# Kernel tuning notes

Measured on AMD Instinct MI355X. Metric: run time of the kernel, lower is better.

The kernel has to match this reference:

```python
import jax, jax.numpy as jnp
import numpy as np

B, F, D = 1024, 160000, 16


def setup_inputs() -> dict:
    key = jax.random.key(0)
    k1, k2, k3 = jax.random.split(key, 3)
    x = jax.random.randint(k1, (B, F), 0, 2, dtype=jnp.int32)  # multi-hot transaction
    emb_w = jax.random.normal(k2, (F, D), dtype=jnp.float32) * 0.05  # FM factor table
    bias_w = jax.random.normal(k3, (F, 1), dtype=jnp.float32) * 0.05  # per-field linear bias
    g_bias = jnp.zeros((), dtype=jnp.float32)  # global bias
    return {"x": x, "emb_w": emb_w, "bias_w": bias_w, "g_bias": g_bias}


def reference(x, emb_w, bias_w, g_bias):
    # mask[b,f] = 1 where field f is active (row > 0 in original tf code)
    mask = (x > 0).astype(emb_w.dtype)  # [B, F]
    # sum of active embeddings per row: equals gather+sum in the original
    ev = mask @ emb_w  # [B, D]
    # sum of squared norms of active embeddings per row
    rowsq = jnp.sum(emb_w * emb_w, axis=1)  # [F]
    sum_sq = mask @ rowsq  # [B]
    # 0.5 * (sum_{i,j} e_i . e_j - sum_i ||e_i||^2) == FM pairwise interaction
    second = 0.5 * (jnp.sum(ev * ev, axis=-1) - sum_sq)  # [B]
    # linear term: global bias + sum of active field biases
    linear = g_bias + mask @ bias_w  # [B, 1]
    return linear + second[:, None]  # [B, 1]
```

## Files before the change

### kernel.cpp

```cpp
#include <hip/hip_runtime.h>
#include <hip/hip_bf16.h>

#define B_ROWS 1024
#define F_FLD  160000
#define D_DIM  16
#define NKB    (F_FLD / 32)
#define NSTAT  (D_DIM + 1)
#define ACC_N  (B_ROWS * NSTAT)
#define CCOLS  6400
#define NGRP   (CCOLS / 256)
#define KBC    (CCOLS / 32)
#define NCHUNK (F_FLD / CCOLS)
#define ROWS_B 16
#define WAVES  8

typedef __attribute__((ext_vector_type(8))) short bf16x8;
typedef __attribute__((ext_vector_type(4))) float f32x4;

static __device__ inline unsigned short f2bf(float x) {
    __hip_bfloat16 h = __float2bfloat16(x);
    union { __hip_bfloat16 h; unsigned short s; } u; u.h = h; return u.s;
}

static __device__ inline bf16x8 expand8(unsigned b) {
    union { unsigned u[4]; bf16x8 v; } r;
    r.u[0] = ((b        & 1u) * 0x3F80u) | (((b >> 1) & 1u) * 0x3F800000u);
    r.u[1] = (((b >> 2) & 1u) * 0x3F80u) | (((b >> 3) & 1u) * 0x3F800000u);
    r.u[2] = (((b >> 4) & 1u) * 0x3F80u) | (((b >> 5) & 1u) * 0x3F800000u);
    r.u[3] = (((b >> 6) & 1u) * 0x3F80u) | (((b >> 7) & 1u) * 0x3F800000u);
    return r.v;
}

__global__ __launch_bounds__(256) void fm_pack(const float* __restrict__ emb,
                                               const float* __restrict__ bias,
                                               unsigned short* __restrict__ embB,
                                               unsigned short* __restrict__ cB2c,
                                               float* __restrict__ acc) {
    const int tid = threadIdx.x;
    const int kb = blockIdx.x * 4 + (tid >> 6);
    const int l = tid & 63, q = l >> 4, n = l & 15;

    float e[8];
    union { unsigned short s[8]; uint4 u; } v;
#pragma unroll
    for (int j = 0; j < 8; ++j) {
        int f = kb * 32 + 4 * j + q;
        e[j] = emb[(size_t)f * D_DIM + n];
        v.s[j] = f2bf(e[j]);
    }
    *(uint4*)(embB + ((size_t)kb * 64 + l) * 8) = v.u;

    union { unsigned short s[8]; uint4 u; } w;
#pragma unroll
    for (int j = 0; j < 8; ++j) {
        float s = e[j] * e[j];
        s += __shfl_xor(s, 1);
        s += __shfl_xor(s, 2);
        s += __shfl_xor(s, 4);
        s += __shfl_xor(s, 8);
        int f = kb * 32 + 4 * j + q;
        w.s[j] = f2bf((n == 0 ? bias[f] : 0.0f) - 0.5f * s);
    }
    if (n == 0) *(uint4*)(cB2c + ((size_t)kb * 4 + q) * 8) = w.u;

    int gid = blockIdx.x * 256 + tid;
    if (gid < ACC_N) acc[gid] = 0.0f;
}

__global__ __launch_bounds__(512, 6) void fm_main(const int* __restrict__ x,
                                                  const unsigned short* __restrict__ embB,
                                                  const unsigned short* __restrict__ cB2c,
                                                  float* __restrict__ acc) {
    __shared__ unsigned long long msk[NGRP][ROWS_B][4];
    __shared__ float red[WAVES][ROWS_B][NSTAT];

    const int tid = threadIdx.x;
    const int w = tid >> 6, l = tid & 63;
    const int q = l >> 4, n = l & 15;
    const int rowbase = blockIdx.y * ROWS_B;
    const int c0 = blockIdx.x * CCOLS;

#pragma unroll
    for (int rr = 0; rr < 2; ++rr) {
        const int rloc = 2 * w + rr;
        const int4* xp = (const int4*)(x + (size_t)(rowbase + rloc) * F_FLD + c0) + l;
        for (int g0 = 0; g0 < NGRP; g0 += 5) {
            int4 v[5];
#pragma unroll
            for (int k = 0; k < 5; ++k) v[k] = xp[(size_t)(g0 + k) * 64];
#pragma unroll
            for (int k = 0; k < 5; ++k) {
                unsigned long long m0 = __ballot(v[k].x > 0);
                unsigned long long m1 = __ballot(v[k].y > 0);
                unsigned long long m2 = __ballot(v[k].z > 0);
                unsigned long long m3 = __ballot(v[k].w > 0);
                if (l == 0) {
                    msk[g0 + k][rloc][0] = m0; msk[g0 + k][rloc][1] = m1;
                    msk[g0 + k][rloc][2] = m2; msk[g0 + k][rloc][3] = m3;
                }
            }
        }
    }
    __syncthreads();

    f32x4 aev = {0.f, 0.f, 0.f, 0.f}, ac = {0.f, 0.f, 0.f, 0.f};
    const uint4* eB = (const uint4*)embB;
    const uint4* cB = (const uint4*)cB2c;
    const int kbg0 = blockIdx.x * KBC;

#pragma unroll 2
    for (int t = 0; t < KBC / WAVES; ++t) {
        const int kb = w * (KBC / WAVES) + t;
        const int g = kb >> 3, byt = kb & 7;
        unsigned long long mv = msk[g][n][q];
        unsigned b = (unsigned)(mv >> (8 * byt)) & 0xFFu;
        bf16x8 A = expand8(b);
        union { uint4 u; bf16x8 v; } Bf, Cf;
        Bf.u = eB[(size_t)(kbg0 + kb) * 64 + l];
        Cf.u = cB[(size_t)(kbg0 + kb) * 4 + q];
        aev = __builtin_amdgcn_mfma_f32_16x16x32_bf16(A, Bf.v, aev, 0, 0, 0);
        ac  = __builtin_amdgcn_mfma_f32_16x16x32_bf16(A, Cf.v, ac,  0, 0, 0);
    }

#pragma unroll
    for (int r = 0; r < 4; ++r) {
        red[w][q * 4 + r][n] = aev[r];
        if (n == 0) red[w][q * 4 + r][16] = ac[r];
    }
    __syncthreads();

    if (tid < ROWS_B * NSTAT) {
        int row = tid / NSTAT, col = tid % NSTAT;
        float s = 0.0f;
#pragma unroll
        for (int ww = 0; ww < WAVES; ++ww) s += red[ww][row][col];
        atomicAdd(acc + (size_t)(rowbase + row) * NSTAT + col, s);
    }
}

__global__ __launch_bounds__(256) void fm_final(const float* __restrict__ acc,
                                                const float* __restrict__ g_bias,
                                                float* __restrict__ out) {
    int row = blockIdx.x * 256 + threadIdx.x;
    if (row >= B_ROWS) return;
    const float* a = acc + (size_t)row * NSTAT;
    float s = 0.0f;
#pragma unroll
    for (int d = 0; d < D_DIM; ++d) s += a[d] * a[d];
    out[row] = g_bias[0] + a[16] + 0.5f * s;
}

extern "C" void kernel_launch(void* const* d_in, const int* in_sizes, int n_in,
                              void* d_out, int out_size, void* d_ws, size_t ws_size,
                              hipStream_t stream) {
    const int*   x      = (const int*)d_in[0];
    const float* emb_w  = (const float*)d_in[1];
    const float* bias_w = (const float*)d_in[2];
    const float* g_bias = (const float*)d_in[3];
    float*       out    = (float*)d_out;

    unsigned short* embB = (unsigned short*)d_ws;
    unsigned short* cB2c = (unsigned short*)((char*)d_ws + (size_t)NKB * 64 * 8 * 2);
    float*          acc  = (float*)((char*)d_ws + (size_t)NKB * 64 * 8 * 2
                                                + (size_t)NKB * 4 * 8 * 2);

    fm_pack<<<dim3(NKB / 4), dim3(256), 0, stream>>>(emb_w, bias_w, embB, cB2c, acc);
    fm_main<<<dim3(NCHUNK, B_ROWS / ROWS_B), dim3(512), 0, stream>>>(x, embB, cB2c, acc);
    fm_final<<<dim3((B_ROWS + 255) / 256), dim3(256), 0, stream>>>(acc, g_bias, out);
}
```

Before: 849.5 us.

## Split mask packing into its own kernel and tile GEMM over 64 rows

The fused kernel is split into two. One kernel reads x with software-prefetched loads and writes packed bitmasks to global memory. A separate GEMM kernel processes 64 rows per block, so each embedding tile is reused across four times as many rows. The atomic accumulation is replaced by per-chunk partial sums that the final kernel reduces, which removes the accumulator zeroing and the atomics. The cost is an extra launch plus a round trip of the mask and partials through global memory.

```diff
diff --git a/kernel.cpp b/kernel.cpp
--- a/kernel.cpp
+++ b/kernel.cpp
@@ -6,13 +6,11 @@
 #define D_DIM  16
 #define NKB    (F_FLD / 32)
 #define NSTAT  (D_DIM + 1)
-#define ACC_N  (B_ROWS * NSTAT)
 #define CCOLS  6400
 #define NGRP   (CCOLS / 256)
 #define KBC    (CCOLS / 32)
 #define NCHUNK (F_FLD / CCOLS)
-#define ROWS_B 16
-#define WAVES  8
+#define MSTRIDE 101
 
 typedef __attribute__((ext_vector_type(8))) short bf16x8;
 typedef __attribute__((ext_vector_type(4))) float f32x4;
@@ -34,8 +32,7 @@
 __global__ __launch_bounds__(256) void fm_pack(const float* __restrict__ emb,
                                                const float* __restrict__ bias,
                                                unsigned short* __restrict__ embB,
-                                               unsigned short* __restrict__ cB2c,
-                                               float* __restrict__ acc) {
+                                               unsigned short* __restrict__ cB2c) {
     const int tid = threadIdx.x;
     const int kb = blockIdx.x * 4 + (tid >> 6);
     const int l = tid & 63, q = l >> 4, n = l & 15;
@@ -62,43 +59,64 @@
         w.s[j] = f2bf((n == 0 ? bias[f] : 0.0f) - 0.5f * s);
     }
     if (n == 0) *(uint4*)(cB2c + ((size_t)kb * 4 + q) * 8) = w.u;
-
-    int gid = blockIdx.x * 256 + tid;
-    if (gid < ACC_N) acc[gid] = 0.0f;
 }
 
-__global__ __launch_bounds__(512, 6) void fm_main(const int* __restrict__ x,
+__global__ __launch_bounds__(512, 6) void fm_mask(const int* __restrict__ x,
+                                                  unsigned long long* __restrict__ maskG) {
+    const int w = threadIdx.x >> 6, l = threadIdx.x & 63;
+    const int row = blockIdx.y * 8 + w;
+    const int ch  = blockIdx.x;
+    const int4* xp = (const int4*)(x + (size_t)row * F_FLD + (size_t)ch * CCOLS) + l;
+    const int gt = l >> 1;
+    const bool odd = l & 1;
+    unsigned long long m0 = 0, m1 = 0;
+
+    int4 v[5], u[5];
+#pragma unroll
+    for (int k = 0; k < 5; ++k) v[k] = xp[k * 64];
+    for (int gb = 0; gb < NGRP; gb += 5) {
+        const bool more = (gb + 5 < NGRP);
+#pragma unroll
+        for (int k = 0; k < 5; ++k) u[k] = more ? xp[(size_t)(gb + 5 + k) * 64] : v[k];
+#pragma unroll
+        for (int k = 0; k < 5; ++k) {
+            unsigned long long b0 = __ballot(v[k].x > 0);
+            unsigned long long b1 = __ballot(v[k].y > 0);
+            unsigned long long b2 = __ballot(v[k].z > 0);
+            unsigned long long b3 = __ballot(v[k].w > 0);
+            if (gb + k == gt) {
+                m0 = odd ? b2 : b0;
+                m1 = odd ? b3 : b1;
+            }
+        }
+#pragma unroll
+        for (int k = 0; k < 5; ++k) v[k] = u[k];
+    }
+    if (l < 50) {
+        union { unsigned long long m[2]; uint4 u; } st;
+        st.m[0] = m0; st.m[1] = m1;
+        *(uint4*)(maskG + ((size_t)row * NCHUNK + ch) * 100 + 2 * l) = st.u;
+    }
+}
+
+__global__ __launch_bounds__(512, 4) void fm_gemm(const unsigned long long* __restrict__ maskG,
                                                   const unsigned short* __restrict__ embB,
                                                   const unsigned short* __restrict__ cB2c,
-                                                  float* __restrict__ acc) {
-    __shared__ unsigned long long msk[NGRP][ROWS_B][4];
-    __shared__ float red[WAVES][ROWS_B][NSTAT];
-
+                                                  float* __restrict__ partial) {
+    __shared__ unsigned long long mlds[64 * MSTRIDE];
+    __shared__ float red[2][4][16][NSTAT];
     const int tid = threadIdx.x;
     const int w = tid >> 6, l = tid & 63;
     const int q = l >> 4, n = l & 15;
-    const int rowbase = blockIdx.y * ROWS_B;
-    const int c0 = blockIdx.x * CCOLS;
+    const int ch = blockIdx.x, rowbase = blockIdx.y * 64;
+    const int mt = w & 3, kh = w >> 2;
 
-#pragma unroll
-    for (int rr = 0; rr < 2; ++rr) {
-        const int rloc = 2 * w + rr;
-        const int4* xp = (const int4*)(x + (size_t)(rowbase + rloc) * F_FLD + c0) + l;
-        for (int g0 = 0; g0 < NGRP; g0 += 5) {
-            int4 v[5];
-#pragma unroll
-            for (int k = 0; k < 5; ++k) v[k] = xp[(size_t)(g0 + k) * 64];
-#pragma unroll
-            for (int k = 0; k < 5; ++k) {
-                unsigned long long m0 = __ballot(v[k].x > 0);
-                unsigned long long m1 = __ballot(v[k].y > 0);
-                unsigned long long m2 = __ballot(v[k].z > 0);
-                unsigned long long m3 = __ballot(v[k].w > 0);
-                if (l == 0) {
-                    msk[g0 + k][rloc][0] = m0; msk[g0 + k][rloc][1] = m1;
-                    msk[g0 + k][rloc][2] = m2; msk[g0 + k][rloc][3] = m3;
-                }
-            }
+    for (int i = 0; i < 13; ++i) {
+        int idx = i * 512 + tid;
+        if (idx < 6400) {
+            int row = idx / 100, wd = idx - row * 100;
+            mlds[row * MSTRIDE + wd] =
+                maskG[((size_t)(rowbase + row) * NCHUNK + ch) * 100 + wd];
         }
     }
     __syncthreads();
@@ -106,48 +124,54 @@
     f32x4 aev = {0.f, 0.f, 0.f, 0.f}, ac = {0.f, 0.f, 0.f, 0.f};
     const uint4* eB = (const uint4*)embB;
     const uint4* cB = (const uint4*)cB2c;
-    const int kbg0 = blockIdx.x * KBC;
+    const int kbase = ch * KBC + kh * 100;
+    const unsigned long long* mrow = mlds + (mt * 16 + n) * MSTRIDE + q;
 
-#pragma unroll 2
-    for (int t = 0; t < KBC / WAVES; ++t) {
-        const int kb = w * (KBC / WAVES) + t;
-        const int g = kb >> 3, byt = kb & 7;
-        unsigned long long mv = msk[g][n][q];
+#pragma unroll 4
+    for (int t = 0; t < 100; ++t) {
+        int kb_local = kh * 100 + t;
+        int g = kb_local >> 3, byt = kb_local & 7;
+        unsigned long long mv = mrow[g * 4];
         unsigned b = (unsigned)(mv >> (8 * byt)) & 0xFFu;
         bf16x8 A = expand8(b);
         union { uint4 u; bf16x8 v; } Bf, Cf;
-        Bf.u = eB[(size_t)(kbg0 + kb) * 64 + l];
-        Cf.u = cB[(size_t)(kbg0 + kb) * 4 + q];
+        Bf.u = eB[(size_t)(kbase + t) * 64 + l];
+        Cf.u = cB[(size_t)(kbase + t) * 4 + q];
         aev = __builtin_amdgcn_mfma_f32_16x16x32_bf16(A, Bf.v, aev, 0, 0, 0);
         ac  = __builtin_amdgcn_mfma_f32_16x16x32_bf16(A, Cf.v, ac,  0, 0, 0);
     }
 
 #pragma unroll
     for (int r = 0; r < 4; ++r) {
-        red[w][q * 4 + r][n] = aev[r];
-        if (n == 0) red[w][q * 4 + r][16] = ac[r];
+        red[kh][mt][q * 4 + r][n] = aev[r];
+        if (n == 0) red[kh][mt][q * 4 + r][16] = ac[r];
     }
     __syncthreads();
 
-    if (tid < ROWS_B * NSTAT) {
-        int row = tid / NSTAT, col = tid % NSTAT;
-        float s = 0.0f;
-#pragma unroll
-        for (int ww = 0; ww < WAVES; ++ww) s += red[ww][row][col];
-        atomicAdd(acc + (size_t)(rowbase + row) * NSTAT + col, s);
+    for (int idx = tid; idx < NSTAT * 64; idx += 512) {
+        int col = idx >> 6, row64 = idx & 63;
+        float s = red[0][row64 >> 4][row64 & 15][col]
+                + red[1][row64 >> 4][row64 & 15][col];
+        partial[((size_t)ch * NSTAT + col) * B_ROWS + rowbase + row64] = s;
     }
 }
 
-__global__ __launch_bounds__(256) void fm_final(const float* __restrict__ acc,
+__global__ __launch_bounds__(256) void fm_final(const float* __restrict__ partial,
                                                 const float* __restrict__ g_bias,
                                                 float* __restrict__ out) {
     int row = blockIdx.x * 256 + threadIdx.x;
-    if (row >= B_ROWS) return;
-    const float* a = acc + (size_t)row * NSTAT;
+    float ev[NSTAT];
+#pragma unroll
+    for (int d = 0; d < NSTAT; ++d) ev[d] = 0.0f;
+    for (int ch = 0; ch < NCHUNK; ++ch) {
+        const float* p = partial + (size_t)ch * NSTAT * B_ROWS + row;
+#pragma unroll
+        for (int d = 0; d < NSTAT; ++d) ev[d] += p[(size_t)d * B_ROWS];
+    }
     float s = 0.0f;
 #pragma unroll
-    for (int d = 0; d < D_DIM; ++d) s += a[d] * a[d];
-    out[row] = g_bias[0] + a[16] + 0.5f * s;
+    for (int d = 0; d < D_DIM; ++d) s += ev[d] * ev[d];
+    out[row] = g_bias[0] + ev[16] + 0.5f * s;
 }
 
 extern "C" void kernel_launch(void* const* d_in, const int* in_sizes, int n_in,
@@ -159,12 +183,14 @@
     const float* g_bias = (const float*)d_in[3];
     float*       out    = (float*)d_out;
 
-    unsigned short* embB = (unsigned short*)d_ws;
-    unsigned short* cB2c = (unsigned short*)((char*)d_ws + (size_t)NKB * 64 * 8 * 2);
-    float*          acc  = (float*)((char*)d_ws + (size_t)NKB * 64 * 8 * 2
-                                                + (size_t)NKB * 4 * 8 * 2);
+    char* p = (char*)d_ws;
+    unsigned short*     embB  = (unsigned short*)p;                 p += (size_t)NKB * 64 * 8 * 2;
+    unsigned short*     cB2c  = (unsigned short*)p;                 p += (size_t)NKB * 4 * 8 * 2;
+    unsigned long long* maskG = (unsigned long long*)p;             p += (size_t)B_ROWS * NCHUNK * 100 * 8;
+    float*              partial = (float*)p;
 
-    fm_pack<<<dim3(NKB / 4), dim3(256), 0, stream>>>(emb_w, bias_w, embB, cB2c, acc);
-    fm_main<<<dim3(NCHUNK, B_ROWS / ROWS_B), dim3(512), 0, stream>>>(x, embB, cB2c, acc);
-    fm_final<<<dim3((B_ROWS + 255) / 256), dim3(256), 0, stream>>>(acc, g_bias, out);
+    fm_pack<<<dim3(NKB / 4), dim3(256), 0, stream>>>(emb_w, bias_w, embB, cB2c);
+    fm_mask<<<dim3(NCHUNK, B_ROWS / 8), dim3(512), 0, stream>>>(x, maskG);
+    fm_gemm<<<dim3(NCHUNK, B_ROWS / 64), dim3(512), 0, stream>>>(maskG, embB, cB2c, partial);
+    fm_final<<<dim3(B_ROWS / 256), dim3(256), 0, stream>>>(partial, g_bias, out);
 }
```

New measurement: 894.8 us. +5.3%, slower.
